# Performance work log

Measured on AMD Instinct MI355X. Metric: run time of the kernel, lower is better.

Reference implementation:

```python
import jax, jax.numpy as jnp
import numpy as np

EPS_SUM = 1e-8
EPS_FILL = 1e-4
NORM_THRESH = 0.1
MASK_THRESH = 0.1


def _shift1(x):
    # conv2d with 1x3 filter [1,1,0], padding (0,1): out[i] = x[i-1] + x[i]
    return x + jnp.pad(x, ((0, 0), (0, 0), (0, 0), (1, 0)))[..., :-1]


def _shift2(x):
    # conv2d with 1x3 filter [0,1,1], padding (0,1): out[i] = x[i] + x[i+1]
    return x + jnp.pad(x, ((0, 0), (0, 0), (0, 0), (0, 1)))[..., 1:]


def _fill(disp, vm, shift_fn, n_steps):
    # Hole filling: each step propagates valid disparity one pixel; after W
    # steps the data-dependent while-loop of the original has converged
    # (further steps are identity), so a fixed-length scan is equivalent.
    def step(carry, _):
        d, m = carry
        m1 = shift_fn(m)
        nm = (m1 > 0).astype(d.dtype)
        d = d * m + shift_fn(d) / (m1 + EPS_FILL) * (nm - m)
        return (d, nm), None
    (disp, vm), _ = jax.lax.scan(step, (disp, vm), None, length=n_steps)
    return disp, vm


def regress_disp(att, valid_mask):
    # att: [B,H,W,W], valid_mask: [B,1,H,W]
    b, h, w, _ = att.shape
    idx = jnp.arange(w, dtype=att.dtype)
    disp_ini = idx[None, None, None, :] - jnp.sum(att * idx, axis=-1).reshape(b, 1, h, w)
    disp = disp_ini * valid_mask
    disp, vm = _fill(disp, valid_mask, _shift1, w)  # left-to-right pass
    disp, vm = _fill(disp, vm, _shift2, w)          # right-to-left pass
    return disp_ini * valid_mask + disp * (1.0 - valid_mask)


def masked_exp_norm(cost, lower):
    # tril/triu-masked exp normalization (non-standard attention)
    tri = jnp.tril if lower else jnp.triu
    c = tri(cost)
    c = jnp.exp(c - jnp.max(c, axis=-1, keepdims=True))
    c = tri(c)
    return c / (jnp.sum(c, axis=-1, keepdims=True) + EPS_SUM)


def gen_pos_shift(w, dtype):
    p = jnp.linspace(0.0, 2.0, w).astype(dtype)
    pos = jnp.maximum(p[:, None] - p[None, :], 0.0)  # pos_l - pos_r, clipped
    return pos[None, None]  # [1,1,W,W]


def gen_raw_disp(att, pos_shift):
    hi = jnp.argmax(att, axis=-1)
    rr = jnp.stack([hi - 1, hi, hi + 1], axis=-1) + 1  # indices into padded axis
    att_pad = jnp.pad(att, ((0, 0), (0, 0), (0, 0), (1, 1)))
    aw = jnp.take_along_axis(att_pad, rr, axis=-1)
    norm = jnp.sum(aw, axis=-1, keepdims=True)
    norm = jnp.where(norm < NORM_THRESH, 1.0, norm)
    aw = aw / norm
    pos_pad = jnp.broadcast_to(jnp.pad(pos_shift, ((0, 0), (0, 0), (0, 0), (1, 1))), att_pad.shape)
    pr = jnp.take_along_axis(pos_pad, rr, axis=-1)
    return jnp.sum(aw * pr, axis=-1)  # [B,H,W]


def setup_inputs() -> dict:
    key = jax.random.key(0)
    k1, k2 = jax.random.split(key)
    B, H, W = 1, 64, 512
    cost1 = jax.random.normal(k1, (B, H, W, W), dtype=jnp.float32)
    cost2 = jax.random.normal(k2, (B, H, W, W), dtype=jnp.float32)
    return {"cost1": cost1, "cost2": cost2}


def reference(cost1, cost2):
    b, h, w, _ = cost1.shape
    att_r2l = masked_exp_norm(cost2, lower=True)   # right-to-left attention
    att_l2r = masked_exp_norm(cost1, lower=False)  # left-to-right attention
    vm_left = (jnp.sum(att_l2r, axis=-2) > MASK_THRESH).astype(cost1.dtype).reshape(b, 1, h, w)
    vm_right = (jnp.sum(att_r2l, axis=-2) > MASK_THRESH).astype(cost1.dtype).reshape(b, 1, h, w)
    disp_r2l = regress_disp(att_r2l, vm_left)   # [B,1,H,W]
    disp_l2r = regress_disp(att_l2r, vm_right)  # [B,1,H,W]
    pos = gen_pos_shift(w, cost1.dtype)
    raw_l2r = gen_raw_disp(att_r2l, pos)                               # [B,H,W]
    raw_r2l = gen_raw_disp(att_l2r, jnp.swapaxes(pos, -1, -2))         # [B,H,W]
    return jnp.concatenate([disp_r2l, disp_l2r, raw_l2r[:, None], raw_r2l[:, None]], axis=1)
```

## Files before the change

kernel.cpp:

```cpp
#include <hip/hip_runtime.h>
#include <float.h>

#define H 64
#define W 512
#define SPLIT 8

__global__ __launch_bounds__(512) void attn_stats_all(
    const float* __restrict__ cost1, const float* __restrict__ cost2,
    float* __restrict__ disp_r2l, float* __restrict__ disp_l2r,
    float* __restrict__ cs_r2l,  float* __restrict__ cs_l2r,
    float* __restrict__ out)
{
  __shared__ float scol[W];
  const int tid  = threadIdx.x;
  const int lane = tid & 63;
  const int wid  = tid >> 6;
  const int gid  = blockIdx.x;
  const bool lower = (gid & 1) == 0;
  const int rest = gid >> 1;
  const int h    = rest / SPLIT;
  const int s    = rest % SPLIT;

  const float* cost = lower ? cost2 : cost1;
  float* disp = lower ? disp_r2l : disp_l2r;
  float* csum = lower ? cs_r2l  : cs_l2r;
  float* raw  = out + (lower ? 2 : 3) * (H * W);

  scol[tid] = 0.f;
  __syncthreads();

  float cacc[8] = {0,0,0,0,0,0,0,0};
  const float pscale = 2.0f / 511.0f;
  const float* hb = cost + (size_t)h * W * W;

  int jmap[8];
  #pragma unroll
  for (int k = 0; k < 8; k++)
    jmap[k] = (k < 4) ? (lane * 4 + k) : (256 + lane * 4 + (k - 4));

  for (int t = wid; t < W / SPLIT; t += 8) {
    const int i = s * (W / SPLIT) + t;
    const float* rp = hb + (size_t)i * W;
    const float4 va = ((const float4*)rp)[lane];
    const float4 vb = ((const float4*)rp)[64 + lane];
    float c[8] = {va.x, va.y, va.z, va.w, vb.x, vb.y, vb.z, vb.w};

    bool vld[8];
    float mxv = -FLT_MAX;
    int   bj  = W;
    #pragma unroll
    for (int k = 0; k < 8; k++) {
      vld[k] = lower ? (jmap[k] <= i) : (jmap[k] >= i);
      if (vld[k] && c[k] > mxv) { mxv = c[k]; bj = jmap[k]; }
    }
    #pragma unroll
    for (int off = 32; off; off >>= 1) {
      const float ov = __shfl_xor(mxv, off);
      const int   oj = __shfl_xor(bj, off);
      if (ov > mxv || (ov == mxv && oj < bj)) { mxv = ov; bj = oj; }
    }
    const int hi = bj;
    float mx = mxv;
    if (lower ? (i < W - 1) : (i > 0)) mx = fmaxf(mx, 0.f);

    float e[8];
    float ssum = 0.f, wsum = 0.f, s0 = 0.f, s1 = 0.f;
    #pragma unroll
    for (int k = 0; k < 8; k++) {
      e[k] = vld[k] ? __expf(c[k] - mx) : 0.f;
      ssum += e[k];
      wsum += e[k] * (float)jmap[k];
      if (jmap[k] >= hi - 1 && jmap[k] <= hi + 1) {
        const float pr = fmaxf((float)(lower ? (i - jmap[k]) : (jmap[k] - i)) * pscale, 0.f);
        s0 += e[k];
        s1 += e[k] * pr;
      }
    }
    #pragma unroll
    for (int off = 32; off; off >>= 1) {
      ssum += __shfl_xor(ssum, off);
      wsum += __shfl_xor(wsum, off);
    }
    const float inv = 1.0f / (ssum + 1e-8f);

    const int jlo = hi > 0 ? hi - 1 : 0;
    const int jh2 = hi < W - 1 ? hi + 1 : W - 1;
    const int l1 = (jlo & 255) >> 2;
    const int l2 = (jh2 & 255) >> 2;
    float t0 = __shfl(s0, l1), t1 = __shfl(s1, l1);
    if (l2 != l1) { t0 += __shfl(s0, l2); t1 += __shfl(s1, l2); }

    #pragma unroll
    for (int k = 0; k < 8; k++) cacc[k] += e[k] * inv;

    if (lane == 0) {
      disp[h * W + i] = (float)i - wsum * inv;
      const float n0 = t0 * inv;
      raw[h * W + i]  = (t1 * inv) / (n0 < 0.1f ? 1.0f : n0);
    }
  }

  #pragma unroll
  for (int k = 0; k < 8; k++) atomicAdd(&scol[jmap[k]], cacc[k]);
  __syncthreads();
  atomicAdd(&csum[h * W + tid], scol[tid]);
}

__global__ __launch_bounds__(64) void fill_rows(
    const float* __restrict__ dispA, const float* __restrict__ csA,
    const float* __restrict__ dispB, const float* __restrict__ csB,
    float* __restrict__ out)
{
  __shared__ float xrow[W];
  const int pair = blockIdx.x >> 6;
  const int h    = blockIdx.x & 63;
  const float* dsp = (pair ? dispB : dispA) + h * W;
  const float* cs  = (pair ? csB  : csA ) + h * W;
  float* o = out + pair * (H * W) + h * W;
  const int lane = threadIdx.x;
  const int j0 = lane * 8;

  float x[8];
  bool m[8];
  int incl[8];
  int run = -1, fv = W;
  #pragma unroll
  for (int k = 0; k < 8; k++) {
    x[k] = dsp[j0 + k];
    m[k] = cs[j0 + k] > 0.1f;
    xrow[j0 + k] = x[k];
    if (m[k]) { run = j0 + k; if (fv == W) fv = j0 + k; }
    incl[k] = run;
  }
  int v = run;
  #pragma unroll
  for (int off = 1; off < 64; off <<= 1) {
    const int tv = __shfl_up(v, off);
    if (lane >= off) v = max(v, tv);
  }
  int excl = __shfl_up(v, 1);
  if (lane == 0) excl = -1;
  int p0 = fv;
  #pragma unroll
  for (int off = 32; off; off >>= 1) p0 = min(p0, __shfl_xor(p0, off));
  __syncthreads();

  const float C2 = -1.4426229e-4f;
  #pragma unroll
  for (int k = 0; k < 8; k++) {
    const int jj = j0 + k;
    float ov;
    if (m[k]) {
      ov = x[k];
    } else {
      const int p = max(excl, incl[k]);
      if (p >= 0)        ov = xrow[p]  * exp2f(C2 * (float)(jj - p));
      else if (p0 < W)   ov = xrow[p0] * exp2f(C2 * (float)(p0 - jj));
      else               ov = 0.f;
    }
    o[jj] = ov;
  }
}

extern "C" void kernel_launch(void* const* d_in, const int* in_sizes, int n_in,
                              void* d_out, int out_size, void* d_ws, size_t ws_size,
                              hipStream_t stream) {
  const float* cost1 = (const float*)d_in[0];
  const float* cost2 = (const float*)d_in[1];
  float* out = (float*)d_out;
  float* w = (float*)d_ws;
  float* disp_r2l_ini = w;
  float* disp_l2r_ini = w + 32768;
  float* cs_l2r       = w + 65536;
  float* cs_r2l       = w + 98304;

  hipMemsetAsync(cs_l2r, 0, 2 * (size_t)H * W * sizeof(float), stream);

  attn_stats_all<<<2 * H * SPLIT, 512, 0, stream>>>(
      cost1, cost2, disp_r2l_ini, disp_l2r_ini, cs_r2l, cs_l2r, out);

  fill_rows<<<2 * H, 64, 0, stream>>>(disp_r2l_ini, cs_l2r,
                                      disp_l2r_ini, cs_r2l, out);
}
```

Baseline: 170.8 us.

## Process four rows per wavefront with 16-lane groups and split shared column sums

Each 64-lane wavefront now handles four rows at once: each 16-lane group owns one row and holds 32 elements per lane, so the reductions need only four shuffle steps instead of six. The column-sum accumulation goes into four padded shared-memory copies, one per lane group, which are summed before the global atomic. The loop over rows shrinks from eight iterations to two per wavefront. In exchange, register pressure rises with 32-element value and accumulator arrays per thread, which may reduce occupancy.

```diff
diff --git a/kernel.cpp b/kernel.cpp
--- a/kernel.cpp
+++ b/kernel.cpp
@@ -11,10 +11,13 @@
     float* __restrict__ cs_r2l,  float* __restrict__ cs_l2r,
     float* __restrict__ out)
 {
-  __shared__ float scol[W];
+  __shared__ float scol[4 * 513];
   const int tid  = threadIdx.x;
   const int lane = tid & 63;
   const int wid  = tid >> 6;
+  const int g    = lane >> 4;
+  const int sub  = lane & 15;
+  const int sub4 = sub * 4;
   const int gid  = blockIdx.x;
   const bool lower = (gid & 1) == 0;
   const int rest = gid >> 1;
@@ -26,35 +29,41 @@
   float* csum = lower ? cs_r2l  : cs_l2r;
   float* raw  = out + (lower ? 2 : 3) * (H * W);
 
-  scol[tid] = 0.f;
+  for (int t = tid; t < 4 * 513; t += 512) scol[t] = 0.f;
   __syncthreads();
 
-  float cacc[8] = {0,0,0,0,0,0,0,0};
+  float cacc[32];
+  #pragma unroll
+  for (int q = 0; q < 32; q++) cacc[q] = 0.f;
+
   const float pscale = 2.0f / 511.0f;
   const float* hb = cost + (size_t)h * W * W;
 
-  int jmap[8];
-  #pragma unroll
-  for (int k = 0; k < 8; k++)
-    jmap[k] = (k < 4) ? (lane * 4 + k) : (256 + lane * 4 + (k - 4));
-
-  for (int t = wid; t < W / SPLIT; t += 8) {
-    const int i = s * (W / SPLIT) + t;
+  for (int t = 0; t < 2; t++) {
+    const int i = s * 64 + t * 32 + wid * 4 + g;
     const float* rp = hb + (size_t)i * W;
-    const float4 va = ((const float4*)rp)[lane];
-    const float4 vb = ((const float4*)rp)[64 + lane];
-    float c[8] = {va.x, va.y, va.z, va.w, vb.x, vb.y, vb.z, vb.w};
-
-    bool vld[8];
+
+    float c[32];
+    #pragma unroll
+    for (int seg = 0; seg < 8; seg++) {
+      const float4 v = ((const float4*)rp)[seg * 16 + sub];
+      c[seg * 4 + 0] = v.x; c[seg * 4 + 1] = v.y;
+      c[seg * 4 + 2] = v.z; c[seg * 4 + 3] = v.w;
+    }
+
     float mxv = -FLT_MAX;
     int   bj  = W;
     #pragma unroll
-    for (int k = 0; k < 8; k++) {
-      vld[k] = lower ? (jmap[k] <= i) : (jmap[k] >= i);
-      if (vld[k] && c[k] > mxv) { mxv = c[k]; bj = jmap[k]; }
-    }
-    #pragma unroll
-    for (int off = 32; off; off >>= 1) {
+    for (int seg = 0; seg < 8; seg++) {
+      #pragma unroll
+      for (int k = 0; k < 4; k++) {
+        const int j = seg * 64 + sub4 + k;
+        const bool vld = lower ? (j <= i) : (j >= i);
+        if (vld && c[seg * 4 + k] > mxv) { mxv = c[seg * 4 + k]; bj = j; }
+      }
+    }
+    #pragma unroll
+    for (int off = 8; off; off >>= 1) {
       const float ov = __shfl_xor(mxv, off);
       const int   oj = __shfl_xor(bj, off);
       if (ov > mxv || (ov == mxv && oj < bj)) { mxv = ov; bj = oj; }
@@ -63,21 +72,26 @@
     float mx = mxv;
     if (lower ? (i < W - 1) : (i > 0)) mx = fmaxf(mx, 0.f);
 
-    float e[8];
     float ssum = 0.f, wsum = 0.f, s0 = 0.f, s1 = 0.f;
     #pragma unroll
-    for (int k = 0; k < 8; k++) {
-      e[k] = vld[k] ? __expf(c[k] - mx) : 0.f;
-      ssum += e[k];
-      wsum += e[k] * (float)jmap[k];
-      if (jmap[k] >= hi - 1 && jmap[k] <= hi + 1) {
-        const float pr = fmaxf((float)(lower ? (i - jmap[k]) : (jmap[k] - i)) * pscale, 0.f);
-        s0 += e[k];
-        s1 += e[k] * pr;
+    for (int seg = 0; seg < 8; seg++) {
+      #pragma unroll
+      for (int k = 0; k < 4; k++) {
+        const int j = seg * 64 + sub4 + k;
+        const bool vld = lower ? (j <= i) : (j >= i);
+        const float e = vld ? __expf(c[seg * 4 + k] - mx) : 0.f;
+        c[seg * 4 + k] = e;
+        ssum += e;
+        wsum += e * (float)j;
+        if (j >= hi - 1 && j <= hi + 1) {
+          const float pr = fmaxf((float)(lower ? (i - j) : (j - i)) * pscale, 0.f);
+          s0 += e;
+          s1 += e * pr;
+        }
       }
     }
     #pragma unroll
-    for (int off = 32; off; off >>= 1) {
+    for (int off = 8; off; off >>= 1) {
       ssum += __shfl_xor(ssum, off);
       wsum += __shfl_xor(wsum, off);
     }
@@ -85,25 +99,31 @@
 
     const int jlo = hi > 0 ? hi - 1 : 0;
     const int jh2 = hi < W - 1 ? hi + 1 : W - 1;
-    const int l1 = (jlo & 255) >> 2;
-    const int l2 = (jh2 & 255) >> 2;
+    const int l1 = (lane & 48) | ((jlo >> 2) & 15);
+    const int l2 = (lane & 48) | ((jh2 >> 2) & 15);
     float t0 = __shfl(s0, l1), t1 = __shfl(s1, l1);
     if (l2 != l1) { t0 += __shfl(s0, l2); t1 += __shfl(s1, l2); }
 
     #pragma unroll
-    for (int k = 0; k < 8; k++) cacc[k] += e[k] * inv;
-
-    if (lane == 0) {
+    for (int q = 0; q < 32; q++) cacc[q] += c[q] * inv;
+
+    if (sub == 0) {
       disp[h * W + i] = (float)i - wsum * inv;
       const float n0 = t0 * inv;
       raw[h * W + i]  = (t1 * inv) / (n0 < 0.1f ? 1.0f : n0);
     }
   }
 
-  #pragma unroll
-  for (int k = 0; k < 8; k++) atomicAdd(&scol[jmap[k]], cacc[k]);
+  float* sc = scol + g * 513;
+  #pragma unroll
+  for (int seg = 0; seg < 8; seg++) {
+    #pragma unroll
+    for (int k = 0; k < 4; k++)
+      atomicAdd(&sc[seg * 64 + sub4 + k], cacc[seg * 4 + k]);
+  }
   __syncthreads();
-  atomicAdd(&csum[h * W + tid], scol[tid]);
+  const float v = scol[tid] + scol[513 + tid] + scol[2 * 513 + tid] + scol[3 * 513 + tid];
+  atomicAdd(&csum[h * W + tid], v);
 }
 
 __global__ __launch_bounds__(64) void fill_rows(
```

New measurement: 235.4 us. 1.38x slower.

## Skip masked triangle chunks and process both attention directions per block

Applied to the files above, without the earlier changes.

Each row now loads only the 64-column chunks on the valid side of the tril/triu mask, so roughly half of each cost matrix is never read or exponentiated. Each block now handles the same 16 rows of both cost tensors, with per-lane column ownership and two shared-memory column-sum buffers. The sub-pixel gather is replaced by full wave reductions of the three-tap sums, with the position term computed algebraically. The trade-off is a larger, divergence-prone unrolled kernel: the number of loaded chunks varies between waves, and it adds more shuffle reductions per row.

```diff
diff --git a/kernel.cpp b/kernel.cpp
--- a/kernel.cpp
+++ b/kernel.cpp
@@ -3,107 +3,158 @@
 
 #define H 64
 #define W 512
-#define SPLIT 8
-
-__global__ __launch_bounds__(512) void attn_stats_all(
+
+__global__ __launch_bounds__(256, 8) void attn_stats_all(
     const float* __restrict__ cost1, const float* __restrict__ cost2,
     float* __restrict__ disp_r2l, float* __restrict__ disp_l2r,
     float* __restrict__ cs_r2l,  float* __restrict__ cs_l2r,
     float* __restrict__ out)
 {
-  __shared__ float scol[W];
+  __shared__ float scol[2][W];
   const int tid  = threadIdx.x;
   const int lane = tid & 63;
   const int wid  = tid >> 6;
-  const int gid  = blockIdx.x;
-  const bool lower = (gid & 1) == 0;
-  const int rest = gid >> 1;
-  const int h    = rest / SPLIT;
-  const int s    = rest % SPLIT;
-
-  const float* cost = lower ? cost2 : cost1;
-  float* disp = lower ? disp_r2l : disp_l2r;
-  float* csum = lower ? cs_r2l  : cs_l2r;
-  float* raw  = out + (lower ? 2 : 3) * (H * W);
-
-  scol[tid] = 0.f;
+  const int b    = blockIdx.x;
+  const int h    = b >> 5;
+  const int slice = b & 31;
+
+  scol[0][tid] = 0.f; scol[0][256 + tid] = 0.f;
+  scol[1][tid] = 0.f; scol[1][256 + tid] = 0.f;
   __syncthreads();
 
-  float cacc[8] = {0,0,0,0,0,0,0,0};
+  float cacc_t[8], cacc_u[8];
+  #pragma unroll
+  for (int c = 0; c < 8; c++) { cacc_t[c] = 0.f; cacc_u[c] = 0.f; }
+
   const float pscale = 2.0f / 511.0f;
-  const float* hb = cost + (size_t)h * W * W;
-
-  int jmap[8];
-  #pragma unroll
-  for (int k = 0; k < 8; k++)
-    jmap[k] = (k < 4) ? (lane * 4 + k) : (256 + lane * 4 + (k - 4));
-
-  for (int t = wid; t < W / SPLIT; t += 8) {
-    const int i = s * (W / SPLIT) + t;
-    const float* rp = hb + (size_t)i * W;
-    const float4 va = ((const float4*)rp)[lane];
-    const float4 vb = ((const float4*)rp)[64 + lane];
-    float c[8] = {va.x, va.y, va.z, va.w, vb.x, vb.y, vb.z, vb.w};
-
-    bool vld[8];
-    float mxv = -FLT_MAX;
-    int   bj  = W;
-    #pragma unroll
-    for (int k = 0; k < 8; k++) {
-      vld[k] = lower ? (jmap[k] <= i) : (jmap[k] >= i);
-      if (vld[k] && c[k] > mxv) { mxv = c[k]; bj = jmap[k]; }
+  const float* baset = cost2 + (size_t)h * W * W;
+  const float* baseu = cost1 + (size_t)h * W * W;
+  float* rawt = out + 2 * H * W;
+  float* rawu = out + 3 * H * W;
+
+  for (int r = 0; r < 4; r++) {
+    const int i  = slice * 16 + r * 4 + wid;
+    const int ci = i >> 6;
+    const int ib = i & 63;
+    const float fi = (float)i;
+
+    {
+      const float* rp = baset + (size_t)i * W;
+      float val[8];
+      float best = -FLT_MAX; int bj = 1024;
+      #pragma unroll
+      for (int c = 0; c < 8; c++) {
+        if (c <= ci) {
+          float v = rp[c * 64 + lane];
+          if (c == ci && lane > ib) v = -FLT_MAX;
+          val[c] = v;
+          if (v > best) { best = v; bj = c * 64 + lane; }
+        }
+      }
+      #pragma unroll
+      for (int off = 32; off; off >>= 1) {
+        const float ov = __shfl_xor(best, off);
+        const int   oj = __shfl_xor(bj, off);
+        if (ov > best || (ov == best && oj < bj)) { best = ov; bj = oj; }
+      }
+      const int hi = bj;
+      const float mx = (i < W - 1) ? fmaxf(best, 0.f) : best;
+      float ssum = 0.f, wsum = 0.f, t0 = 0.f, w0 = 0.f;
+      #pragma unroll
+      for (int c = 0; c < 8; c++) {
+        if (c <= ci) {
+          const float e = __expf(val[c] - mx);
+          val[c] = e;
+          const int j = c * 64 + lane;
+          const float p = e * (float)j;
+          ssum += e; wsum += p;
+          if ((unsigned)(j - (hi - 1)) <= 2u) { t0 += e; w0 += p; }
+        }
+      }
+      #pragma unroll
+      for (int off = 32; off; off >>= 1) {
+        ssum += __shfl_xor(ssum, off);
+        wsum += __shfl_xor(wsum, off);
+        t0   += __shfl_xor(t0, off);
+        w0   += __shfl_xor(w0, off);
+      }
+      const float inv = 1.f / (ssum + 1e-8f);
+      #pragma unroll
+      for (int c = 0; c < 8; c++)
+        if (c <= ci) cacc_t[c] += val[c] * inv;
+      if (lane == 0) {
+        disp_r2l[h * W + i] = fi - wsum * inv;
+        const float n0 = t0 * inv;
+        const float t1 = pscale * (fi * t0 - w0);
+        rawt[h * W + i] = (t1 * inv) / (n0 < 0.1f ? 1.f : n0);
+      }
     }
-    #pragma unroll
-    for (int off = 32; off; off >>= 1) {
-      const float ov = __shfl_xor(mxv, off);
-      const int   oj = __shfl_xor(bj, off);
-      if (ov > mxv || (ov == mxv && oj < bj)) { mxv = ov; bj = oj; }
+
+    {
+      const float* rp = baseu + (size_t)i * W;
+      float val[8];
+      float best = -FLT_MAX; int bj = 1024;
+      #pragma unroll
+      for (int c = 0; c < 8; c++) {
+        if (c >= ci) {
+          float v = rp[c * 64 + lane];
+          if (c == ci && lane < ib) v = -FLT_MAX;
+          val[c] = v;
+          if (v > best) { best = v; bj = c * 64 + lane; }
+        }
+      }
+      #pragma unroll
+      for (int off = 32; off; off >>= 1) {
+        const float ov = __shfl_xor(best, off);
+        const int   oj = __shfl_xor(bj, off);
+        if (ov > best || (ov == best && oj < bj)) { best = ov; bj = oj; }
+      }
+      const int hi = bj;
+      const float mx = (i > 0) ? fmaxf(best, 0.f) : best;
+      float ssum = 0.f, wsum = 0.f, t0 = 0.f, w0 = 0.f;
+      #pragma unroll
+      for (int c = 0; c < 8; c++) {
+        if (c >= ci) {
+          const float e = __expf(val[c] - mx);
+          val[c] = e;
+          const int j = c * 64 + lane;
+          const float p = e * (float)j;
+          ssum += e; wsum += p;
+          if ((unsigned)(j - (hi - 1)) <= 2u) { t0 += e; w0 += p; }
+        }
+      }
+      #pragma unroll
+      for (int off = 32; off; off >>= 1) {
+        ssum += __shfl_xor(ssum, off);
+        wsum += __shfl_xor(wsum, off);
+        t0   += __shfl_xor(t0, off);
+        w0   += __shfl_xor(w0, off);
+      }
+      const float inv = 1.f / (ssum + 1e-8f);
+      #pragma unroll
+      for (int c = 0; c < 8; c++)
+        if (c >= ci) cacc_u[c] += val[c] * inv;
+      if (lane == 0) {
+        disp_l2r[h * W + i] = fi - wsum * inv;
+        const float n0 = t0 * inv;
+        const float t1 = pscale * (w0 - fi * t0);
+        rawu[h * W + i] = (t1 * inv) / (n0 < 0.1f ? 1.f : n0);
+      }
     }
-    const int hi = bj;
-    float mx = mxv;
-    if (lower ? (i < W - 1) : (i > 0)) mx = fmaxf(mx, 0.f);
-
-    float e[8];
-    float ssum = 0.f, wsum = 0.f, s0 = 0.f, s1 = 0.f;
-    #pragma unroll
-    for (int k = 0; k < 8; k++) {
-      e[k] = vld[k] ? __expf(c[k] - mx) : 0.f;
-      ssum += e[k];
-      wsum += e[k] * (float)jmap[k];
-      if (jmap[k] >= hi - 1 && jmap[k] <= hi + 1) {
-        const float pr = fmaxf((float)(lower ? (i - jmap[k]) : (jmap[k] - i)) * pscale, 0.f);
-        s0 += e[k];
-        s1 += e[k] * pr;
-      }
-    }
-    #pragma unroll
-    for (int off = 32; off; off >>= 1) {
-      ssum += __shfl_xor(ssum, off);
-      wsum += __shfl_xor(wsum, off);
-    }
-    const float inv = 1.0f / (ssum + 1e-8f);
-
-    const int jlo = hi > 0 ? hi - 1 : 0;
-    const int jh2 = hi < W - 1 ? hi + 1 : W - 1;
-    const int l1 = (jlo & 255) >> 2;
-    const int l2 = (jh2 & 255) >> 2;
-    float t0 = __shfl(s0, l1), t1 = __shfl(s1, l1);
-    if (l2 != l1) { t0 += __shfl(s0, l2); t1 += __shfl(s1, l2); }
-
-    #pragma unroll
-    for (int k = 0; k < 8; k++) cacc[k] += e[k] * inv;
-
-    if (lane == 0) {
-      disp[h * W + i] = (float)i - wsum * inv;
-      const float n0 = t0 * inv;
-      raw[h * W + i]  = (t1 * inv) / (n0 < 0.1f ? 1.0f : n0);
-    }
-  }
-
-  #pragma unroll
-  for (int k = 0; k < 8; k++) atomicAdd(&scol[jmap[k]], cacc[k]);
+  }
+
+  #pragma unroll
+  for (int c = 0; c < 8; c++) {
+    atomicAdd(&scol[0][c * 64 + lane], cacc_t[c]);
+    atomicAdd(&scol[1][c * 64 + lane], cacc_u[c]);
+  }
   __syncthreads();
-  atomicAdd(&csum[h * W + tid], scol[tid]);
+  #pragma unroll
+  for (int q = 0; q < 2; q++) {
+    const int col = q * 256 + tid;
+    atomicAdd(&cs_r2l[h * W + col], scol[0][col]);
+    atomicAdd(&cs_l2r[h * W + col], scol[1][col]);
+  }
 }
 
 __global__ __launch_bounds__(64) void fill_rows(
@@ -176,7 +227,7 @@
 
   hipMemsetAsync(cs_l2r, 0, 2 * (size_t)H * W * sizeof(float), stream);
 
-  attn_stats_all<<<2 * H * SPLIT, 512, 0, stream>>>(
+  attn_stats_all<<<2 * H * 16, 256, 0, stream>>>(
       cost1, cost2, disp_r2l_ini, disp_l2r_ini, cs_r2l, cs_l2r, out);
 
   fill_rows<<<2 * H, 64, 0, stream>>>(disp_r2l_ini, cs_l2r,
```

Measured after the change: 213.7 us. 25.2% more time.

## Split attention stats into online-softmax row pass and log-sum-exp column pass

Applied to the files above, without the earlier changes.

Replaces the single wave-per-row stats kernel with a row kernel that assigns four threads per row. Each thread computes an online softmax max/sum/weighted sum and tracks the argmax with its neighbours, and the quarters are merged by shuffles. A second kernel re-reads the cost volume and recomputes normalized exponentials from stored log-sum-exp values to build column sums as per-quarter partials. This removes the global atomics and the memset, but reads the 128MB input twice instead of once, so the gain depends on whether the row kernel's better ALU use outweighs the extra memory traffic.

```diff
diff --git a/kernel.cpp b/kernel.cpp
--- a/kernel.cpp
+++ b/kernel.cpp
@@ -3,133 +3,218 @@
 
 #define H 64
 #define W 512
-#define SPLIT 8
-
-__global__ __launch_bounds__(512) void attn_stats_all(
+#define L2E 1.4426950408889634f
+
+#define WS_DISPT 0
+#define WS_DISPU 32768
+#define WS_AEXP  65536
+#define WS_PART  131072
+
+__global__ __launch_bounds__(256, 8) void row_stats(
     const float* __restrict__ cost1, const float* __restrict__ cost2,
-    float* __restrict__ disp_r2l, float* __restrict__ disp_l2r,
-    float* __restrict__ cs_r2l,  float* __restrict__ cs_l2r,
-    float* __restrict__ out)
+    float* __restrict__ ws, float* __restrict__ out)
 {
-  __shared__ float scol[W];
-  const int tid  = threadIdx.x;
-  const int lane = tid & 63;
-  const int wid  = tid >> 6;
-  const int gid  = blockIdx.x;
-  const bool lower = (gid & 1) == 0;
-  const int rest = gid >> 1;
-  const int h    = rest / SPLIT;
-  const int s    = rest % SPLIT;
-
-  const float* cost = lower ? cost2 : cost1;
-  float* disp = lower ? disp_r2l : disp_l2r;
-  float* csum = lower ? cs_r2l  : cs_l2r;
-  float* raw  = out + (lower ? 2 : 3) * (H * W);
-
-  scol[tid] = 0.f;
+  const int g   = blockIdx.x * 256 + threadIdx.x;
+  const int row = g >> 2;
+  const int q   = g & 3;
+  const int tn  = row & 1;
+  const int rr  = row >> 1;
+  const int h   = rr >> 9;
+  const int i   = rr & 511;
+  const bool lower = (tn == 0);
+  const float* base = (lower ? cost2 : cost1) + ((size_t)h * W + i) * W + q * 128;
+  const int j0 = q * 128;
+
+  float m = -FLT_MAX, s = 0.f, w = 0.f;
+  float best = -FLT_MAX, vp = -FLT_MAX, vn = -FLT_MAX;
+  int   bj = 0;
+  float firstV = 0.f, lastprev = -FLT_MAX;
+  bool  pend = false;
+
+  for (int cc = 0; cc < 8; cc++) {
+    float c[16];
+    const float4* p4 = (const float4*)(base + cc * 16);
+    #pragma unroll
+    for (int t = 0; t < 4; t++) {
+      const float4 v = p4[t];
+      c[t*4+0]=v.x; c[t*4+1]=v.y; c[t*4+2]=v.z; c[t*4+3]=v.w;
+    }
+    const int jc = j0 + cc * 16;
+    #pragma unroll
+    for (int k = 0; k < 16; k++) {
+      const int j = jc + k;
+      const bool v = lower ? (j <= i) : (j >= i);
+      c[k] = v ? c[k] : -FLT_MAX;
+    }
+    if (cc == 0) firstV = c[0];
+    vn = pend ? c[0] : vn;
+    pend = false;
+    float cm = c[0];
+    #pragma unroll
+    for (int k = 1; k < 16; k++) cm = fmaxf(cm, c[k]);
+    #pragma unroll
+    for (int k = 0; k < 16; k++) {
+      const bool upd = c[k] > best;
+      if (upd) {
+        best = c[k]; bj = jc + k;
+        vp = (k == 0) ? lastprev : c[k-1];
+        if (k < 15) vn = c[k+1]; else pend = true;
+      }
+    }
+    lastprev = c[15];
+    float cs = 0.f, cw = 0.f;
+    #pragma unroll
+    for (int k = 0; k < 16; k++) {
+      const float e = exp2f((c[k] - cm) * L2E);
+      cs += e;
+      cw = fmaf((float)k, e, cw);
+    }
+    cw = fmaf((float)jc, cs, cw);
+    const float mn = fmaxf(m, cm);
+    const float fa = exp2f((m - mn) * L2E);
+    const float fb = exp2f((cm - mn) * L2E);
+    s = s * fa + cs * fb;
+    w = w * fa + cw * fb;
+    m = mn;
+  }
+  float lastV = lastprev;
+
+  #pragma unroll
+  for (int off = 1; off <= 2; off <<= 1) {
+    const float om = __shfl_xor(m, off);
+    const float os = __shfl_xor(s, off);
+    const float ow = __shfl_xor(w, off);
+    const float ob = __shfl_xor(best, off);
+    const int   oj = __shfl_xor(bj, off);
+    const float ovp = __shfl_xor(vp, off);
+    const float ovn = __shfl_xor(vn, off);
+    const float ofv = __shfl_xor(firstV, off);
+    const float olv = __shfl_xor(lastV, off);
+    const float mn = fmaxf(m, om);
+    const float fa = exp2f((m - mn) * L2E);
+    const float fb = exp2f((om - mn) * L2E);
+    s = s * fa + os * fb;
+    w = w * fa + ow * fb;
+    m = mn;
+    const bool hi = (q & off) != 0;
+    const int pj0 = (q & ~(2 * off - 1)) * 128;
+    const int alj = pj0 + off * 128 - 1;
+    const int bfj = alj + 1;
+    const float Ab = hi ? ob : best, Bb = hi ? best : ob;
+    const int   Aj = hi ? oj : bj,   Bj = hi ? bj : oj;
+    const float Avp = hi ? ovp : vp, Bvp = hi ? vp : ovp;
+    const float Avn = hi ? ovn : vn, Bvn = hi ? vn : ovn;
+    const float Afv = hi ? ofv : firstV, Bfv = hi ? firstV : ofv;
+    const float Alv = hi ? olv : lastV,  Blv = hi ? lastV : olv;
+    const bool tb = Bb > Ab;
+    best = tb ? Bb : Ab;
+    bj   = tb ? Bj : Aj;
+    vp   = tb ? ((Bj == bfj) ? Alv : Bvp) : Avp;
+    vn   = tb ? Bvn : ((Aj == alj) ? Bfv : Avn);
+    firstV = Afv; lastV = Blv;
+  }
+
+  if (q == 0) {
+    const float pscale = 2.0f / 511.0f;
+    const bool hasMasked = lower ? (i < W - 1) : (i > 0);
+    const float mx = hasMasked ? fmaxf(m, 0.f) : m;
+    const float fsc = exp2f((m - mx) * L2E);
+    s *= fsc; w *= fsc;
+    const float inv = 1.f / (s + 1e-8f);
+    float* disp = ws + (lower ? WS_DISPT : WS_DISPU);
+    disp[(h << 9) + i] = (float)i - w * inv;
+    ws[WS_AEXP + (tn << 15) + (h << 9) + i] = fmaf(mx, L2E, log2f(s + 1e-8f));
+    const float e_h = fsc;
+    const float e_p = exp2f((vp - mx) * L2E);
+    const float e_n = exp2f((vn - mx) * L2E);
+    const float t0 = e_p + e_h + e_n;
+    const float fb = (float)bj;
+    const float w0 = fmaf(e_p, fb - 1.f, fmaf(e_h, fb, e_n * (fb + 1.f)));
+    const float fi = (float)i;
+    const float t1 = pscale * (lower ? (fi * t0 - w0) : (w0 - fi * t0));
+    const float n0 = t0 * inv;
+    float* raw = out + (lower ? 2 : 3) * (H * W);
+    raw[(h << 9) + i] = (t1 * inv) / (n0 < 0.1f ? 1.f : n0);
+  }
+}
+
+__global__ __launch_bounds__(512) void col_sums(
+    const float* __restrict__ cost1, const float* __restrict__ cost2,
+    float* __restrict__ ws)
+{
+  __shared__ float sa[128];
+  __shared__ float sc[4][516];
+  const int bb = blockIdx.x;
+  const int tn = bb & 1;
+  const int rest = bb >> 1;
+  const int h  = rest >> 2;
+  const int qb = rest & 3;
+  const bool lower = (tn == 0);
+  const float* base = (lower ? cost2 : cost1) + (size_t)h * W * W;
+  const int tid = threadIdx.x;
+  const int rg = tid >> 7;
+  const int ct = tid & 127;
+  const int jj = ct * 4;
+
+  if (tid < 128) sa[tid] = ws[WS_AEXP + (tn << 15) + (h << 9) + qb * 128 + tid];
   __syncthreads();
 
-  float cacc[8] = {0,0,0,0,0,0,0,0};
-  const float pscale = 2.0f / 511.0f;
-  const float* hb = cost + (size_t)h * W * W;
-
-  int jmap[8];
-  #pragma unroll
-  for (int k = 0; k < 8; k++)
-    jmap[k] = (k < 4) ? (lane * 4 + k) : (256 + lane * 4 + (k - 4));
-
-  for (int t = wid; t < W / SPLIT; t += 8) {
-    const int i = s * (W / SPLIT) + t;
-    const float* rp = hb + (size_t)i * W;
-    const float4 va = ((const float4*)rp)[lane];
-    const float4 vb = ((const float4*)rp)[64 + lane];
-    float c[8] = {va.x, va.y, va.z, va.w, vb.x, vb.y, vb.z, vb.w};
-
-    bool vld[8];
-    float mxv = -FLT_MAX;
-    int   bj  = W;
-    #pragma unroll
-    for (int k = 0; k < 8; k++) {
-      vld[k] = lower ? (jmap[k] <= i) : (jmap[k] >= i);
-      if (vld[k] && c[k] > mxv) { mxv = c[k]; bj = jmap[k]; }
-    }
-    #pragma unroll
-    for (int off = 32; off; off >>= 1) {
-      const float ov = __shfl_xor(mxv, off);
-      const int   oj = __shfl_xor(bj, off);
-      if (ov > mxv || (ov == mxv && oj < bj)) { mxv = ov; bj = oj; }
-    }
-    const int hi = bj;
-    float mx = mxv;
-    if (lower ? (i < W - 1) : (i > 0)) mx = fmaxf(mx, 0.f);
-
-    float e[8];
-    float ssum = 0.f, wsum = 0.f, s0 = 0.f, s1 = 0.f;
-    #pragma unroll
-    for (int k = 0; k < 8; k++) {
-      e[k] = vld[k] ? __expf(c[k] - mx) : 0.f;
-      ssum += e[k];
-      wsum += e[k] * (float)jmap[k];
-      if (jmap[k] >= hi - 1 && jmap[k] <= hi + 1) {
-        const float pr = fmaxf((float)(lower ? (i - jmap[k]) : (jmap[k] - i)) * pscale, 0.f);
-        s0 += e[k];
-        s1 += e[k] * pr;
-      }
-    }
-    #pragma unroll
-    for (int off = 32; off; off >>= 1) {
-      ssum += __shfl_xor(ssum, off);
-      wsum += __shfl_xor(wsum, off);
-    }
-    const float inv = 1.0f / (ssum + 1e-8f);
-
-    const int jlo = hi > 0 ? hi - 1 : 0;
-    const int jh2 = hi < W - 1 ? hi + 1 : W - 1;
-    const int l1 = (jlo & 255) >> 2;
-    const int l2 = (jh2 & 255) >> 2;
-    float t0 = __shfl(s0, l1), t1 = __shfl(s1, l1);
-    if (l2 != l1) { t0 += __shfl(s0, l2); t1 += __shfl(s1, l2); }
-
-    #pragma unroll
-    for (int k = 0; k < 8; k++) cacc[k] += e[k] * inv;
-
-    if (lane == 0) {
-      disp[h * W + i] = (float)i - wsum * inv;
-      const float n0 = t0 * inv;
-      raw[h * W + i]  = (t1 * inv) / (n0 < 0.1f ? 1.0f : n0);
-    }
-  }
-
-  #pragma unroll
-  for (int k = 0; k < 8; k++) atomicAdd(&scol[jmap[k]], cacc[k]);
+  float4 acc = {0.f, 0.f, 0.f, 0.f};
+  const int r0 = qb * 128 + rg * 32;
+  #pragma unroll 4
+  for (int t = 0; t < 32; t++) {
+    const int r = r0 + t;
+    const float a = sa[rg * 32 + t];
+    const float4 v = *(const float4*)(base + (size_t)r * W + jj);
+    const float x0 = exp2f(fmaf(v.x, L2E, -a));
+    const float x1 = exp2f(fmaf(v.y, L2E, -a));
+    const float x2 = exp2f(fmaf(v.z, L2E, -a));
+    const float x3 = exp2f(fmaf(v.w, L2E, -a));
+    if (lower) {
+      acc.x += (jj     <= r) ? x0 : 0.f;
+      acc.y += (jj + 1 <= r) ? x1 : 0.f;
+      acc.z += (jj + 2 <= r) ? x2 : 0.f;
+      acc.w += (jj + 3 <= r) ? x3 : 0.f;
+    } else {
+      acc.x += (jj     >= r) ? x0 : 0.f;
+      acc.y += (jj + 1 >= r) ? x1 : 0.f;
+      acc.z += (jj + 2 >= r) ? x2 : 0.f;
+      acc.w += (jj + 3 >= r) ? x3 : 0.f;
+    }
+  }
+  *(float4*)&sc[rg][jj] = acc;
   __syncthreads();
-  atomicAdd(&csum[h * W + tid], scol[tid]);
+  if (tid < 512) {
+    const float p = sc[0][tid] + sc[1][tid] + sc[2][tid] + sc[3][tid];
+    ws[WS_PART + (((tn * H + h) * 4 + qb) << 9) + tid] = p;
+  }
 }
 
 __global__ __launch_bounds__(64) void fill_rows(
-    const float* __restrict__ dispA, const float* __restrict__ csA,
-    const float* __restrict__ dispB, const float* __restrict__ csB,
-    float* __restrict__ out)
+    const float* __restrict__ ws, float* __restrict__ out)
 {
   __shared__ float xrow[W];
   const int pair = blockIdx.x >> 6;
   const int h    = blockIdx.x & 63;
-  const float* dsp = (pair ? dispB : dispA) + h * W;
-  const float* cs  = (pair ? csB  : csA ) + h * W;
+  const float* dsp = ws + (pair ? WS_DISPU : WS_DISPT) + h * W;
+  const int cstn = pair ? 0 : 1;
+  const float* pb = ws + WS_PART + (((cstn * H + h) * 4) << 9);
   float* o = out + pair * (H * W) + h * W;
   const int lane = threadIdx.x;
   const int j0 = lane * 8;
 
   float x[8];
-  bool m[8];
+  bool mvals[8];
   int incl[8];
   int run = -1, fv = W;
   #pragma unroll
   for (int k = 0; k < 8; k++) {
-    x[k] = dsp[j0 + k];
-    m[k] = cs[j0 + k] > 0.1f;
-    xrow[j0 + k] = x[k];
-    if (m[k]) { run = j0 + k; if (fv == W) fv = j0 + k; }
+    const int jj = j0 + k;
+    x[k] = dsp[jj];
+    const float cs = pb[jj] + pb[512 + jj] + pb[1024 + jj] + pb[1536 + jj];
+    mvals[k] = cs > 0.1f;
+    xrow[jj] = x[k];
+    if (mvals[k]) { run = jj; if (fv == W) fv = jj; }
     incl[k] = run;
   }
   int v = run;
@@ -150,7 +235,7 @@
   for (int k = 0; k < 8; k++) {
     const int jj = j0 + k;
     float ov;
-    if (m[k]) {
+    if (mvals[k]) {
       ov = x[k];
     } else {
       const int p = max(excl, incl[k]);
@@ -168,17 +253,9 @@
   const float* cost1 = (const float*)d_in[0];
   const float* cost2 = (const float*)d_in[1];
   float* out = (float*)d_out;
-  float* w = (float*)d_ws;
-  float* disp_r2l_ini = w;
-  float* disp_l2r_ini = w + 32768;
-  float* cs_l2r       = w + 65536;
-  float* cs_r2l       = w + 98304;
-
-  hipMemsetAsync(cs_l2r, 0, 2 * (size_t)H * W * sizeof(float), stream);
-
-  attn_stats_all<<<2 * H * SPLIT, 512, 0, stream>>>(
-      cost1, cost2, disp_r2l_ini, disp_l2r_ini, cs_r2l, cs_l2r, out);
-
-  fill_rows<<<2 * H, 64, 0, stream>>>(disp_r2l_ini, cs_l2r,
-                                      disp_l2r_ini, cs_r2l, out);
-}
+  float* ws = (float*)d_ws;
+
+  row_stats<<<1024, 256, 0, stream>>>(cost1, cost2, ws, out);
+  col_sums<<<512, 512, 0, stream>>>(cost1, cost2, ws);
+  fill_rows<<<2 * H, 64, 0, stream>>>(ws, out);
+}
```

After: 227.8 us. 1.33x slower.
